# Optimization experiments

Hardware: AMD Instinct MI355X
Metric: run time of the kernel (lower is better)

The kernel has to match this reference:

```python
import jax, jax.numpy as jnp
import numpy as np

B, H, W, C, NH, WS, DEPTH = 32, 56, 56, 192, 6, 7, 2
SHIFTS = (0, WS // 2)
N = WS * WS
NW = (H // WS) * (W // WS)
HD = C // NH
SCALE = HD ** -0.5


def _rel_index():
    coords = np.stack(np.meshgrid(np.arange(WS), np.arange(WS), indexing='ij')).reshape(2, -1)
    rel = (coords[:, :, None] - coords[:, None, :]).transpose(1, 2, 0)
    rel[..., 0] += WS - 1
    rel[..., 1] += WS - 1
    rel[..., 0] *= 2 * WS - 1
    return jnp.asarray(rel.sum(-1))  # (N, N) int

REL_IDX = _rel_index()


def _attn_mask():
    # BasicLayer.creat_mask for the shifted block (shift = WS//2)
    img = np.zeros((H, W))
    sl = (slice(0, -WS), slice(-WS, -SHIFTS[1]), slice(-SHIFTS[1], None))
    cnt = 0
    for hs in sl:
        for ws_ in sl:
            img[hs, ws_] = cnt
            cnt += 1
    mw = img.reshape(H // WS, WS, W // WS, WS).transpose(0, 2, 1, 3).reshape(-1, N)
    d = mw[:, None, :] - mw[:, :, None]  # unsqueeze(1) - unsqueeze(2)
    return jnp.asarray(np.where(d != 0, -100.0, 0.0).astype(np.float32))  # (NW, N, N)

ATTN_MASK = _attn_mask()


def _ln(x, w, b):
    mu = x.mean(-1, keepdims=True)
    var = ((x - mu) ** 2).mean(-1, keepdims=True)
    return (x - mu) * jax.lax.rsqrt(var + 1e-5) * w + b


def _block(x, p, shift):
    Bn, L, Cc = x.shape
    shortcut = x
    h = _ln(x, p['n1w'], p['n1b']).reshape(Bn, H, W, Cc)
    if shift > 0:
        h = jnp.roll(h, (-shift, -shift), axis=(1, 2))
    # window_partition -> (Bn*NW, N, C)
    h = h.reshape(Bn, H // WS, WS, W // WS, WS, Cc).transpose(0, 1, 3, 2, 4, 5).reshape(-1, N, Cc)
    qkv = (h @ p['qkvw'].T + p['qkvb']).reshape(-1, N, 3, NH, HD).transpose(2, 0, 3, 1, 4)
    q, k, v = qkv[0] * SCALE, qkv[1], qkv[2]  # (Bw, NH, N, HD)
    attn = jnp.einsum('bhnd,bhmd->bhnm', q, k)
    bias = p['rpb'][REL_IDX].transpose(2, 0, 1)  # (NH, N, N)
    attn = attn + bias[None]
    if shift > 0:
        attn = attn.reshape(Bn, NW, NH, N, N) + ATTN_MASK[None, :, None]
        attn = attn.reshape(-1, NH, N, N)
    attn = jax.nn.softmax(attn, axis=-1)
    h = jnp.einsum('bhnm,bhmd->bhnd', attn, v).transpose(0, 2, 1, 3).reshape(-1, N, Cc)
    h = h @ p['projw'].T + p['projb']
    # window_reverse
    h = h.reshape(Bn, H // WS, W // WS, WS, WS, Cc).transpose(0, 1, 3, 2, 4, 5).reshape(Bn, H, W, Cc)
    if shift > 0:
        # NOTE: source rolls back by window_size (not shift_size); replicated faithfully
        h = jnp.roll(h, (WS, WS), axis=(1, 2))
    x = shortcut + h.reshape(Bn, L, Cc)
    m = _ln(x, p['n2w'], p['n2b'])
    m = jax.nn.gelu(m @ p['f1w'].T + p['f1b'], approximate=False) @ p['f2w'].T + p['f2b']
    return x + m


def setup_inputs() -> dict:
    key = jax.random.key(0)
    ks = jax.random.split(key, 15)
    r = lambda k, s, sc: jax.random.normal(k, s, dtype=jnp.float32) * sc
    return {
        'x': r(ks[0], (B, H * W, C), 1.0),
        'n1w': 1.0 + r(ks[1], (DEPTH, C), 0.01),
        'n1b': r(ks[2], (DEPTH, C), 0.01),
        'qkvw': r(ks[3], (DEPTH, 3 * C, C), 0.05),
        'qkvb': r(ks[4], (DEPTH, 3 * C), 0.01),
        'rpb': r(ks[5], (DEPTH, (2 * WS - 1) ** 2, NH), 0.02),
        'projw': r(ks[6], (DEPTH, C, C), 0.05),
        'projb': r(ks[7], (DEPTH, C), 0.01),
        'n2w': 1.0 + r(ks[8], (DEPTH, C), 0.01),
        'n2b': r(ks[9], (DEPTH, C), 0.01),
        'f1w': r(ks[10], (DEPTH, 4 * C, C), 0.05),
        'f1b': r(ks[11], (DEPTH, 4 * C), 0.01),
        'f2w': r(ks[12], (DEPTH, C, 4 * C), 0.05),
        'f2b': r(ks[13], (DEPTH, C), 0.01),
    }


def reference(x, n1w, n1b, qkvw, qkvb, rpb, projw, projb, n2w, n2b, f1w, f1b, f2w, f2b):
    for i in range(DEPTH):
        p = {'n1w': n1w[i], 'n1b': n1b[i], 'qkvw': qkvw[i], 'qkvb': qkvb[i],
             'rpb': rpb[i], 'projw': projw[i], 'projb': projb[i],
             'n2w': n2w[i], 'n2b': n2b[i], 'f1w': f1w[i], 'f1b': f1b[i],
             'f2w': f2w[i], 'f2b': f2b[i]}
        x = _block(x, p, SHIFTS[i])
    return x
```

## Files before the change

### kernel.cpp

```cpp
#include <hip/hip_runtime.h>
#include <hip/hip_bf16.h>
#include <math.h>

typedef __hip_bfloat16 bf16;

#define BB    32
#define HH    56
#define WWI   56
#define CC    192
#define NHH   6
#define WSS   7
#define NN    49
#define NWIN  64
#define HDD   32
#define LL    (HH*WWI)
#define ROWS  (BB*NWIN*NN)
#define TOT   ((size_t)ROWS*CC)
#define SCALEQ 0.17677669529663687f

#define OFF_N1W   0
#define OFF_N1B   384
#define OFF_QKVW  768
#define OFF_QKVB  221952
#define OFF_RPB   223104
#define OFF_PROJW 225132
#define OFF_PROJB 298860
#define OFF_N2W   299244
#define OFF_N2B   299628
#define OFF_F1W   300012
#define OFF_F1B   594924
#define OFF_F2W   596460
#define OFF_F2B   891372

typedef __bf16 bf16x8v __attribute__((ext_vector_type(8)));
typedef float  f32x4   __attribute__((ext_vector_type(4)));

__device__ __forceinline__ float tof(bf16 v){ return __bfloat162float(v); }
__device__ __forceinline__ bf16  tob(float v){ return __float2bfloat16(v); }
__device__ __forceinline__ float xload(const float* p){ return *p; }
__device__ __forceinline__ float xload(const bf16*  p){ return tof(*p); }
__device__ __forceinline__ void  xstore(float* p, float v){ *p = v; }
__device__ __forceinline__ void  xstore(bf16*  p, float v){ *p = tob(v); }

__device__ __forceinline__ bf16x8v ldfrag(const bf16* p){
    return *(const bf16x8v*)p;
}
__device__ __forceinline__ unsigned short bfbits(float v){
    bf16 b = tob(v);
    return __builtin_bit_cast(unsigned short, b);
}
__device__ __forceinline__ bf16 mkbf(unsigned short u){
    return __builtin_bit_cast(bf16, u);
}

__device__ __forceinline__ float fast_gelu(float x){
    float u = fabsf(x) * 0.70710678118f;
    float t = __builtin_amdgcn_rcpf(1.f + 0.3275911f*u);
    float p = t*(0.254829592f + t*(-0.284496736f + t*(1.421413741f +
              t*(-1.453152027f + t*1.061405429f))));
    float e = __expf(-u*u);
    float erfu = 1.f - p*e;
    float s = copysignf(erfu, x);
    return 0.5f*x*(1.f + s);
}

__global__ void k_detect(const unsigned short* __restrict__ w, int* __restrict__ flag){
    if (blockIdx.x == 0 && threadIdx.x == 0){
        int cnt = 0;
        for (int k = 0; k < 16; ++k){
            unsigned short u = w[2*k];
            if (u >= 0x3E00 && u <= 0x4100) ++cnt;
        }
        *flag = (cnt >= 8) ? 1 : 0;
    }
}

__global__ void k_canon(const void* __restrict__ src, bf16* __restrict__ dst,
                        int n, const int* __restrict__ flag){
    int i = blockIdx.x * blockDim.x + threadIdx.x;
    if (i >= n) return;
    if (*flag) dst[i] = ((const bf16*)src)[i];
    else       dst[i] = tob(((const float*)src)[i]);
}

template<typename XT>
__global__ void k_convert_in(const void* __restrict__ in, XT* __restrict__ X,
                             const int* __restrict__ flag){
    size_t i = (size_t)blockIdx.x * blockDim.x + threadIdx.x;
    if (i >= TOT) return;
    float v = (*flag) ? tof(((const bf16*)in)[i]) : ((const float*)in)[i];
    xstore(&X[i], v);
}

template<typename XT>
__global__ void k_out(const XT* __restrict__ X, void* __restrict__ out,
                      const int* __restrict__ flag){
    size_t i = (size_t)blockIdx.x * blockDim.x + threadIdx.x;
    if (i >= TOT) return;
    float v = xload(&X[i]);
    if (*flag) ((bf16*)out)[i] = tob(v);
    else       ((float*)out)[i] = v;
}

template<typename XT>
__global__ __launch_bounds__(256) void k_ln_part(const XT* __restrict__ X,
        const bf16* __restrict__ w, const bf16* __restrict__ bsh,
        bf16* __restrict__ Hwin, int shift){
    int wv = threadIdx.x >> 6, lane = threadIdx.x & 63;
    int row = blockIdx.x*4 + wv;
    int b   = row / (NWIN*NN);
    int win = (row / NN) % NWIN;
    int n   = row % NN;
    int wh = win >> 3, ww = win & 7;
    int iy = n / WSS, ix = n % WSS;
    int sy = (wh*WSS + iy + shift) % HH;
    int sx = (ww*WSS + ix + shift) % WWI;
    const XT* src = X + ((size_t)(b*LL + sy*WWI + sx))*CC;
    float v0 = xload(&src[lane]);
    float v1 = xload(&src[lane+64]);
    float v2 = xload(&src[lane+128]);
    float sm  = v0+v1+v2;
    float sm2 = v0*v0+v1*v1+v2*v2;
    #pragma unroll
    for (int st = 1; st < 64; st <<= 1){
        sm  += __shfl_xor(sm,  st);
        sm2 += __shfl_xor(sm2, st);
    }
    float mu  = sm * (1.f/CC);
    float inv = rsqrtf(sm2*(1.f/CC) - mu*mu + 1e-5f);
    bf16* dst = Hwin + (size_t)row*CC;
    dst[lane]     = tob((v0-mu)*inv*tof(w[lane])     + tof(bsh[lane]));
    dst[lane+64]  = tob((v1-mu)*inv*tof(w[lane+64])  + tof(bsh[lane+64]));
    dst[lane+128] = tob((v2-mu)*inv*tof(w[lane+128]) + tof(bsh[lane+128]));
}

__device__ __forceinline__ int mt0(int i){ return (i < 3) ? i*16 : 33; }

__global__ __launch_bounds__(512, 4) void k_attn(const bf16* __restrict__ Hwin,
        const bf16* __restrict__ qkvw, const bf16* __restrict__ qkvb,
        const bf16* __restrict__ rpb, bf16* __restrict__ AOut, int masked){
    __shared__ bf16 smem[31104];
    bf16* qls = smem;
    bf16* kls = smem + 9408;
    bf16* vT  = smem + 18816;
    bf16* Pls = smem;

    int t = threadIdx.x;
    int win  = blockIdx.x;
    int winl = win & (NWIN-1);
    int wh = winl >> 3, ww = winl & 7;
    int wv = t >> 6, lane = t & 63;
    int li16 = lane & 15, quad = lane >> 4;

    for (int idx = t; idx < 192*15; idx += 512){
        int d = idx / 15, tokp = 49 + idx % 15;
        vT[d*64 + (tokp ^ ((d&7)<<3))] = tob(0.f);
    }

    {
        int p = wv & 1, c = wv >> 1;
        int m0a = mt0(2*p), m0b = mt0(2*p+1);
        const bf16* hg = Hwin + (size_t)win*NN*CC;
        bf16x8v afa[6], afb[6];
        #pragma unroll
        for (int kc = 0; kc < 6; ++kc){
            afa[kc] = ldfrag(hg + (m0a+li16)*CC + kc*32 + quad*8);
            afb[kc] = ldfrag(hg + (m0b+li16)*CC + kc*32 + quad*8);
        }
        #pragma unroll 3
        for (int j = 0; j < 9; ++j){
            int nt = c + 4*j;
            int col = nt*16 + li16;
            f32x4 acc0 = {0.f,0.f,0.f,0.f}, acc1 = {0.f,0.f,0.f,0.f};
            #pragma unroll
            for (int kc = 0; kc < 6; ++kc){
                bf16x8v bfr = ldfrag(qkvw + (size_t)col*CC + kc*32 + quad*8);
                acc0 = __builtin_amdgcn_mfma_f32_16x16x32_bf16(afa[kc], bfr, acc0, 0, 0, 0);
                acc1 = __builtin_amdgcn_mfma_f32_16x16x32_bf16(afb[kc], bfr, acc1, 0, 0, 0);
            }
            float bias = tof(qkvb[col]);
            int m  = col / CC;
            int cm = col - m*CC;
            #pragma unroll
            for (int r = 0; r < 4; ++r){
                int rowA = m0a + quad*4 + r;
                int rowB = m0b + quad*4 + r;
                float v0 = acc0[r] + bias, v1 = acc1[r] + bias;
                if (m == 0){
                    qls[rowA*CC + (cm ^ ((rowA&7)<<3))] = tob(v0*SCALEQ);
                    qls[rowB*CC + (cm ^ ((rowB&7)<<3))] = tob(v1*SCALEQ);
                } else if (m == 1){
                    kls[rowA*CC + (cm ^ ((rowA&7)<<3))] = tob(v0);
                    kls[rowB*CC + (cm ^ ((rowB&7)<<3))] = tob(v1);
                } else {
                    vT[cm*64 + (rowA ^ ((cm&7)<<3))] = tob(v0);
                    vT[cm*64 + (rowB ^ ((cm&7)<<3))] = tob(v1);
                }
            }
        }
    }
    __syncthreads();

    unsigned int pk[3][8];
    #pragma unroll
    for (int j = 0; j < 3; ++j){
        int id = wv + 8*j;
        int mt = id & 3, h = id >> 2;
        int m0 = mt0(mt);
        int rowq = m0 + li16;
        bf16x8v afr = ldfrag(qls + rowq*CC + ((h*32 + quad*8) ^ ((rowq&7)<<3)));
        f32x4 s[4];
        #pragma unroll
        for (int nt = 0; nt < 4; ++nt){
            int rowk = nt*16 + li16;
            bf16x8v bfr = ldfrag(kls + rowk*CC + ((h*32 + quad*8) ^ ((rowk&7)<<3)));
            f32x4 z = {0.f,0.f,0.f,0.f};
            s[nt] = __builtin_amdgcn_mfma_f32_16x16x32_bf16(afr, bfr, z, 0, 0, 0);
        }
        #pragma unroll
        for (int nt = 0; nt < 4; ++nt){
            int jj = nt*16 + li16;
            int valid = (jj < NN);
            int jc = valid ? jj : 48;
            int yj = (jc*37) >> 8, xj = jc - 7*yj;
            int lj = 0;
            if (masked){
                int ayj = wh*WSS + yj, axj = ww*WSS + xj;
                lj = ((ayj<49)?0:(ayj<53)?1:2)*3 + ((axj<49)?0:(axj<53)?1:2);
            }
            #pragma unroll
            for (int r = 0; r < 4; ++r){
                int i = m0 + quad*4 + r;
                int yi = (i*37) >> 8, xi = i - 7*yi;
                int ridx = (yi - yj + 6)*13 + (xi - xj + 6);
                float v = s[nt][r] + tof(rpb[ridx*NHH + h]);
                if (masked){
                    int ayi = wh*WSS + yi, axi = ww*WSS + xi;
                    int li = ((ayi<49)?0:(ayi<53)?1:2)*3 + ((axi<49)?0:(axi<53)?1:2);
                    if (li != lj) v -= 100.f;
                }
                s[nt][r] = valid ? v : -1e30f;
            }
        }
        float mx[4], sm[4];
        #pragma unroll
        for (int r = 0; r < 4; ++r)
            mx[r] = fmaxf(fmaxf(s[0][r], s[1][r]), fmaxf(s[2][r], s[3][r]));
        #pragma unroll
        for (int st = 1; st < 16; st <<= 1){
            #pragma unroll
            for (int r = 0; r < 4; ++r) mx[r] = fmaxf(mx[r], __shfl_xor(mx[r], st));
        }
        #pragma unroll
        for (int nt = 0; nt < 4; ++nt){
            #pragma unroll
            for (int r = 0; r < 4; ++r) s[nt][r] = __expf(s[nt][r] - mx[r]);
        }
        #pragma unroll
        for (int r = 0; r < 4; ++r) sm[r] = (s[0][r]+s[1][r]) + (s[2][r]+s[3][r]);
        #pragma unroll
        for (int st = 1; st < 16; st <<= 1){
            #pragma unroll
            for (int r = 0; r < 4; ++r) sm[r] += __shfl_xor(sm[r], st);
        }
        #pragma unroll
        for (int r = 0; r < 4; ++r) sm[r] = 1.f / sm[r];
        #pragma unroll
        for (int nt = 0; nt < 4; ++nt){
            #pragma unroll
            for (int rr = 0; rr < 2; ++rr){
                unsigned int u0 = bfbits(s[nt][2*rr]   * sm[2*rr]);
                unsigned int u1 = bfbits(s[nt][2*rr+1] * sm[2*rr+1]);
                pk[j][nt*2+rr] = (u1 << 16) | u0;
            }
        }
    }
    __syncthreads();

    #pragma unroll
    for (int j = 0; j < 3; ++j){
        int id = wv + 8*j;
        int m0 = mt0(id & 3), h = id >> 2;
        #pragma unroll
        for (int nt = 0; nt < 4; ++nt){
            int jj = nt*16 + li16;
            #pragma unroll
            for (int rr = 0; rr < 2; ++rr){
                unsigned int u = pk[j][nt*2+rr];
                int tok0 = m0 + quad*4 + 2*rr;
                int tok1 = tok0 + 1;
                Pls[(h*NN + tok0)*64 + (jj ^ ((tok0&7)<<3))] = mkbf((unsigned short)(u & 0xffff));
                Pls[(h*NN + tok1)*64 + (jj ^ ((tok1&7)<<3))] = mkbf((unsigned short)(u >> 16));
            }
        }
    }
    __syncthreads();

    {
        int mt = wv & 3, nto = wv >> 2;
        int m0 = mt0(mt), n0 = nto*16;
        #pragma unroll
        for (int h = 0; h < NHH; ++h){
            f32x4 acc = {0.f,0.f,0.f,0.f};
            #pragma unroll
            for (int kc = 0; kc < 2; ++kc){
                int rowp = m0 + li16;
                bf16x8v afr = ldfrag(Pls + (h*NN + rowp)*64 + ((kc*32 + quad*8) ^ ((rowp&7)<<3)));
                int rowv = h*HDD + n0 + li16;
                bf16x8v bfr = ldfrag(vT + rowv*64 + ((kc*32 + quad*8) ^ ((rowv&7)<<3)));
                acc = __builtin_amdgcn_mfma_f32_16x16x32_bf16(afr, bfr, acc, 0, 0, 0);
            }
            #pragma unroll
            for (int r = 0; r < 4; ++r){
                int tok = m0 + quad*4 + r;
                AOut[(size_t)win*NN*CC + tok*CC + h*HDD + n0 + li16] = tob(acc[r]);
            }
        }
    }
}

#define AS_STRIDE 200
template<typename XT>
__global__ __launch_bounds__(256) void k_proj_res(const bf16* __restrict__ AOut,
        const bf16* __restrict__ pw, const bf16* __restrict__ pb,
        XT* __restrict__ X, int shift){
    __shared__ bf16 as[32*AS_STRIDE];
    int t = threadIdx.x;
    int row0 = blockIdx.x * 32;
    for (int idx = t; idx < 32*CC; idx += 256){
        int r = idx / CC, c = idx % CC;
        as[r*AS_STRIDE + c] = AOut[(size_t)(row0 + r)*CC + c];
    }
    __syncthreads();
    int wv = t >> 6, lane = t & 63;
    int li16 = lane & 15, quad = lane >> 4;
    int roll = (shift > 0) ? WSS : 0;
    for (int nt = 0; nt < 3; ++nt){
        int n0 = wv*48 + nt*16;
        int col = n0 + li16;
        bf16x8v bfr[6];
        #pragma unroll
        for (int kc = 0; kc < 6; ++kc)
            bfr[kc] = ldfrag(pw + (size_t)col*CC + kc*32 + quad*8);
        float bias = tof(pb[col]);
        for (int mt = 0; mt < 2; ++mt){
            int m0 = mt*16;
            f32x4 acc = {0.f,0.f,0.f,0.f};
            #pragma unroll
            for (int kc = 0; kc < 6; ++kc){
                bf16x8v afr = ldfrag(as + (m0 + li16)*AS_STRIDE + kc*32 + quad*8);
                acc = __builtin_amdgcn_mfma_f32_16x16x32_bf16(afr, bfr[kc], acc, 0, 0, 0);
            }
            #pragma unroll
            for (int r = 0; r < 4; ++r){
                int grow = row0 + m0 + quad*4 + r;
                int b   = grow / (NWIN*NN);
                int rem = grow % (NWIN*NN);
                int win = rem / NN;
                int n   = rem % NN;
                int wh = win >> 3, ww = win & 7;
                int iy = n / WSS, ix = n % WSS;
                int y = (wh*WSS + iy + roll) % HH;
                int x = (ww*WSS + ix + roll) % WWI;
                size_t idx = ((size_t)(b*LL + y*WWI + x))*CC + col;
                xstore(&X[idx], xload(&X[idx]) + acc[r] + bias);
            }
        }
    }
}

template<typename XT>
__global__ __launch_bounds__(256, 4) void k_mlp(XT* __restrict__ X,
        const bf16* __restrict__ n2w, const bf16* __restrict__ n2b,
        const bf16* __restrict__ w1, const bf16* __restrict__ b1,
        const bf16* __restrict__ w2, const bf16* __restrict__ b2){
    __shared__ bf16  xin[32*192];
    __shared__ bf16  h1h[32*384];
    __shared__ float part[256], part2[256];
    __shared__ float stats[64];
    int t = threadIdx.x;
    size_t row0 = (size_t)blockIdx.x * 32;

    float vals[24];
    int r8 = t >> 3, s8 = t & 7;
    {
        const XT* xr = X + (row0 + r8)*CC + s8*24;
        if constexpr (sizeof(XT) == 4){
            #pragma unroll
            for (int q = 0; q < 6; ++q){
                float4 f = *(const float4*)((const float*)xr + q*4);
                vals[q*4+0]=f.x; vals[q*4+1]=f.y; vals[q*4+2]=f.z; vals[q*4+3]=f.w;
            }
        } else {
            #pragma unroll
            for (int q = 0; q < 3; ++q){
                bf16x8v f = ldfrag((const bf16*)xr + q*8);
                #pragma unroll
                for (int e = 0; e < 8; ++e) vals[q*8+e] = tof(mkbf(__builtin_bit_cast(unsigned short, f[e])));
            }
        }
        float sm = 0.f, sm2 = 0.f;
        #pragma unroll
        for (int c = 0; c < 24; ++c){ sm += vals[c]; sm2 += vals[c]*vals[c]; }
        part[t] = sm; part2[t] = sm2;
    }
    __syncthreads();
    if (t < 32){
        float s = 0.f, s2 = 0.f;
        #pragma unroll
        for (int k = 0; k < 8; ++k){ s += part[t*8+k]; s2 += part2[t*8+k]; }
        float mu  = s * (1.f/CC);
        float var = s2 * (1.f/CC) - mu*mu;
        stats[t]      = mu;
        stats[32 + t] = rsqrtf(var + 1e-5f);
    }
    __syncthreads();
    {
        float mu = stats[r8], inv = stats[32+r8];
        #pragma unroll
        for (int c = 0; c < 24; ++c){
            int col = s8*24 + c;
            xin[r8*192 + (col ^ ((r8&7)<<3))] =
                tob((vals[c]-mu)*inv*tof(n2w[col]) + tof(n2b[col]));
        }
    }
    __syncthreads();

    int wv = t >> 6, lane = t & 63;
    int li16 = lane & 15, quad = lane >> 4;
    int sw = (li16 & 7) << 3;

    bf16x8v afr0[6], afr1[6];
    #pragma unroll
    for (int kc = 0; kc < 6; ++kc){
        afr0[kc] = ldfrag(xin + (0  + li16)*192 + ((kc*32 + quad*8) ^ sw));
        afr1[kc] = ldfrag(xin + (16 + li16)*192 + ((kc*32 + quad*8) ^ sw));
    }

    f32x4 acc2[3][2];
    #pragma unroll
    for (int nt = 0; nt < 3; ++nt){
        acc2[nt][0] = (f32x4){0.f,0.f,0.f,0.f};
        acc2[nt][1] = (f32x4){0.f,0.f,0.f,0.f};
    }

    #pragma unroll
    for (int half = 0; half < 2; ++half){
        #pragma unroll 2
        for (int nt6 = 0; nt6 < 6; ++nt6){
            int cl  = (wv*6 + nt6)*16 + li16;
            int col = half*384 + cl;
            bf16x8v bfr[6];
            #pragma unroll
            for (int kc = 0; kc < 6; ++kc)
                bfr[kc] = ldfrag(w1 + (size_t)col*CC + kc*32 + quad*8);
            float bb = tof(b1[col]);
            f32x4 acA = {0.f,0.f,0.f,0.f}, acB = {0.f,0.f,0.f,0.f};
            #pragma unroll
            for (int kc = 0; kc < 6; ++kc){
                acA = __builtin_amdgcn_mfma_f32_16x16x32_bf16(afr0[kc], bfr[kc], acA, 0, 0, 0);
                acB = __builtin_amdgcn_mfma_f32_16x16x32_bf16(afr1[kc], bfr[kc], acB, 0, 0, 0);
            }
            #pragma unroll
            for (int r = 0; r < 4; ++r){
                int rowA = quad*4 + r, rowB = 16 + quad*4 + r;
                h1h[rowA*384 + (cl ^ ((rowA&7)<<3))] = tob(fast_gelu(acA[r] + bb));
                h1h[rowB*384 + (cl ^ ((rowB&7)<<3))] = tob(fast_gelu(acB[r] + bb));
            }
        }
        __syncthreads();
        #pragma unroll 4
        for (int kc = 0; kc < 12; ++kc){
            int kg = half*12 + kc;
            bf16x8v a0 = ldfrag(h1h + (0  + li16)*384 + ((kc*32 + quad*8) ^ sw));
            bf16x8v a1 = ldfrag(h1h + (16 + li16)*384 + ((kc*32 + quad*8) ^ sw));
            #pragma unroll
            for (int nt = 0; nt < 3; ++nt){
                int col = wv*48 + nt*16 + li16;
                bf16x8v bfr = ldfrag(w2 + (size_t)col*768 + kg*32 + quad*8);
                acc2[nt][0] = __builtin_amdgcn_mfma_f32_16x16x32_bf16(a0, bfr, acc2[nt][0], 0, 0, 0);
                acc2[nt][1] = __builtin_amdgcn_mfma_f32_16x16x32_bf16(a1, bfr, acc2[nt][1], 0, 0, 0);
            }
        }
        __syncthreads();
    }

    #pragma unroll
    for (int nt = 0; nt < 3; ++nt){
        int col = wv*48 + nt*16 + li16;
        float bias = tof(b2[col]);
        #pragma unroll
        for (int r = 0; r < 4; ++r){
            size_t i0 = (row0 + 0  + quad*4 + r)*CC + col;
            size_t i1 = (row0 + 16 + quad*4 + r)*CC + col;
            xstore(&X[i0], xload(&X[i0]) + acc2[nt][0][r] + bias);
            xstore(&X[i1], xload(&X[i1]) + acc2[nt][1][r] + bias);
        }
    }
}

template<typename XT>
static void run_pipeline(const bf16* wb, const void* xin, int* flag,
                         XT* X, bf16* Hwin, bf16* AOut, void* out,
                         hipStream_t stream){
    k_convert_in<XT><<<(int)(TOT/256), 256, 0, stream>>>(xin, X, flag);
    for (int i = 0; i < 2; ++i){
        int shift = i ? (WSS/2) : 0;
        k_ln_part<XT><<<ROWS/4, 256, 0, stream>>>(X, wb+OFF_N1W + i*CC,
                wb+OFF_N1B + i*CC, Hwin, shift);
        k_attn<<<BB*NWIN, 512, 0, stream>>>(Hwin,
                wb+OFF_QKVW + (size_t)i*3*CC*CC, wb+OFF_QKVB + (size_t)i*3*CC,
                wb+OFF_RPB + (size_t)i*169*NHH, AOut, i);
        k_proj_res<XT><<<ROWS/32, 256, 0, stream>>>(AOut,
                wb+OFF_PROJW + (size_t)i*CC*CC, wb+OFF_PROJB + i*CC, X, shift);
        k_mlp<XT><<<ROWS/32, 256, 0, stream>>>(X,
                wb+OFF_N2W + i*CC, wb+OFF_N2B + i*CC,
                wb+OFF_F1W + (size_t)i*4*CC*CC, wb+OFF_F1B + (size_t)i*4*CC,
                wb+OFF_F2W + (size_t)i*CC*4*CC, wb+OFF_F2B + i*CC);
    }
    k_out<XT><<<(int)(TOT/256), 256, 0, stream>>>(X, out, flag);
}

extern "C" void kernel_launch(void* const* d_in, const int* in_sizes, int n_in,
                              void* d_out, int out_size, void* d_ws, size_t ws_size,
                              hipStream_t stream){
    char* p = (char*)d_ws;
    int*  flag = (int*)p;
    bf16* wb   = (bf16*)(p + 16);
    char* q    = p + 16 + (2u<<20);

    k_detect<<<1, 64, 0, stream>>>((const unsigned short*)d_in[1], flag);

    static const int widx[13] = {1,2,3,4,5,6,7,8,9,10,11,12,13};
    static const int woff[13] = {OFF_N1W,OFF_N1B,OFF_QKVW,OFF_QKVB,OFF_RPB,
                                 OFF_PROJW,OFF_PROJB,OFF_N2W,OFF_N2B,
                                 OFF_F1W,OFF_F1B,OFF_F2W,OFF_F2B};
    static const int wsz[13]  = {384,384,221184,1152,2028,73728,384,384,384,
                                 294912,1536,294912,384};
    for (int k = 0; k < 13; ++k)
        k_canon<<<(wsz[k]+255)/256, 256, 0, stream>>>(d_in[widx[k]], wb+woff[k],
                                                      wsz[k], flag);

    size_t needF32 = 16 + (2u<<20) + TOT*4 + TOT*2 + TOT*2;
    if (ws_size >= needF32){
        float* X   = (float*)q;       q += TOT*4;
        bf16* Hwin = (bf16*)q;        q += TOT*2;
        bf16* AOut = (bf16*)q;
        run_pipeline<float>(wb, d_in[0], flag, X, Hwin, AOut, d_out, stream);
    } else {
        bf16* X    = (bf16*)q;        q += TOT*2;
        bf16* Hwin = (bf16*)q;        q += TOT*2;
        bf16* AOut = (bf16*)q;
        run_pipeline<bf16>(wb, d_in[0], flag, X, Hwin, AOut, d_out, stream);
    }
}
```

Baseline: 1.202 ms.

## Retile fused MLP kernel to 64-row blocks with four hidden-dimension passes

The fused LayerNorm+MLP kernel now processes 64 rows per block instead of 32. The hidden dimension is split into four 192-wide passes, each staged through a 64x192 shared buffer. Every weight fragment loaded from global memory now feeds four MFMA row tiles instead of two, halving the weight traffic per row. LayerNorm is computed per wave with shuffle reductions instead of shared-memory partial sums. This costs more registers (accumulators are 3x4 per wave), a lower occupancy target, and half as many blocks in the grid.

```diff
diff --git a/kernel.cpp b/kernel.cpp
--- a/kernel.cpp
+++ b/kernel.cpp
@@ -370,131 +370,119 @@
 }
 
 template<typename XT>
-__global__ __launch_bounds__(256, 4) void k_mlp(XT* __restrict__ X,
+__global__ __launch_bounds__(256, 3) void k_mlp(XT* __restrict__ X,
         const bf16* __restrict__ n2w, const bf16* __restrict__ n2b,
         const bf16* __restrict__ w1, const bf16* __restrict__ b1,
         const bf16* __restrict__ w2, const bf16* __restrict__ b2){
-    __shared__ bf16  xin[32*192];
-    __shared__ bf16  h1h[32*384];
-    __shared__ float part[256], part2[256];
-    __shared__ float stats[64];
+    __shared__ bf16 xin[64*192];
+    __shared__ bf16 h1p[64*192];
     int t = threadIdx.x;
-    size_t row0 = (size_t)blockIdx.x * 32;
-
-    float vals[24];
-    int r8 = t >> 3, s8 = t & 7;
-    {
-        const XT* xr = X + (row0 + r8)*CC + s8*24;
-        if constexpr (sizeof(XT) == 4){
-            #pragma unroll
-            for (int q = 0; q < 6; ++q){
-                float4 f = *(const float4*)((const float*)xr + q*4);
-                vals[q*4+0]=f.x; vals[q*4+1]=f.y; vals[q*4+2]=f.z; vals[q*4+3]=f.w;
-            }
-        } else {
-            #pragma unroll
-            for (int q = 0; q < 3; ++q){
-                bf16x8v f = ldfrag((const bf16*)xr + q*8);
-                #pragma unroll
-                for (int e = 0; e < 8; ++e) vals[q*8+e] = tof(mkbf(__builtin_bit_cast(unsigned short, f[e])));
-            }
-        }
-        float sm = 0.f, sm2 = 0.f;
-        #pragma unroll
-        for (int c = 0; c < 24; ++c){ sm += vals[c]; sm2 += vals[c]*vals[c]; }
-        part[t] = sm; part2[t] = sm2;
-    }
-    __syncthreads();
-    if (t < 32){
-        float s = 0.f, s2 = 0.f;
-        #pragma unroll
-        for (int k = 0; k < 8; ++k){ s += part[t*8+k]; s2 += part2[t*8+k]; }
-        float mu  = s * (1.f/CC);
-        float var = s2 * (1.f/CC) - mu*mu;
-        stats[t]      = mu;
-        stats[32 + t] = rsqrtf(var + 1e-5f);
-    }
-    __syncthreads();
-    {
-        float mu = stats[r8], inv = stats[32+r8];
-        #pragma unroll
-        for (int c = 0; c < 24; ++c){
-            int col = s8*24 + c;
-            xin[r8*192 + (col ^ ((r8&7)<<3))] =
-                tob((vals[c]-mu)*inv*tof(n2w[col]) + tof(n2b[col]));
-        }
-    }
-    __syncthreads();
-
     int wv = t >> 6, lane = t & 63;
     int li16 = lane & 15, quad = lane >> 4;
+    size_t row0 = (size_t)blockIdx.x * 64;
+
+    {
+        float nw0 = tof(n2w[lane]), nw1 = tof(n2w[lane+64]), nw2 = tof(n2w[lane+128]);
+        float nb0 = tof(n2b[lane]), nb1 = tof(n2b[lane+64]), nb2 = tof(n2b[lane+128]);
+        #pragma unroll 4
+        for (int i = 0; i < 16; ++i){
+            int r = wv*16 + i;
+            const XT* xr = X + (row0 + r)*CC;
+            float v0 = xload(&xr[lane]);
+            float v1 = xload(&xr[lane+64]);
+            float v2 = xload(&xr[lane+128]);
+            float sm  = v0+v1+v2;
+            float sm2 = v0*v0+v1*v1+v2*v2;
+            #pragma unroll
+            for (int st = 1; st < 64; st <<= 1){
+                sm  += __shfl_xor(sm,  st);
+                sm2 += __shfl_xor(sm2, st);
+            }
+            float mu  = sm * (1.f/CC);
+            float inv = rsqrtf(sm2*(1.f/CC) - mu*mu + 1e-5f);
+            int swz = (r&7)<<3;
+            bf16* xrow = xin + r*192;
+            xrow[lane        ^ swz] = tob((v0-mu)*inv*nw0 + nb0);
+            xrow[(lane+64)   ^ swz] = tob((v1-mu)*inv*nw1 + nb1);
+            xrow[(lane+128)  ^ swz] = tob((v2-mu)*inv*nw2 + nb2);
+        }
+    }
+    __syncthreads();
+
     int sw = (li16 & 7) << 3;
-
-    bf16x8v afr0[6], afr1[6];
+    f32x4 acc2[3][4];
     #pragma unroll
-    for (int kc = 0; kc < 6; ++kc){
-        afr0[kc] = ldfrag(xin + (0  + li16)*192 + ((kc*32 + quad*8) ^ sw));
-        afr1[kc] = ldfrag(xin + (16 + li16)*192 + ((kc*32 + quad*8) ^ sw));
-    }
-
-    f32x4 acc2[3][2];
+    for (int j = 0; j < 3; ++j)
+        #pragma unroll
+        for (int m = 0; m < 4; ++m)
+            acc2[j][m] = (f32x4){0.f,0.f,0.f,0.f};
+
+    for (int pass = 0; pass < 4; ++pass){
+        f32x4 a1[3][4];
+        #pragma unroll
+        for (int j = 0; j < 3; ++j)
+            #pragma unroll
+            for (int m = 0; m < 4; ++m)
+                a1[j][m] = (f32x4){0.f,0.f,0.f,0.f};
+        #pragma unroll
+        for (int kc = 0; kc < 6; ++kc){
+            bf16x8v af[4];
+            #pragma unroll
+            for (int m = 0; m < 4; ++m)
+                af[m] = ldfrag(xin + (m*16 + li16)*192 + ((kc*32 + quad*8) ^ sw));
+            #pragma unroll
+            for (int j = 0; j < 3; ++j){
+                int col = pass*192 + (wv*3 + j)*16 + li16;
+                bf16x8v bfr = ldfrag(w1 + (size_t)col*CC + kc*32 + quad*8);
+                #pragma unroll
+                for (int m = 0; m < 4; ++m)
+                    a1[j][m] = __builtin_amdgcn_mfma_f32_16x16x32_bf16(af[m], bfr, a1[j][m], 0, 0, 0);
+            }
+        }
+        #pragma unroll
+        for (int j = 0; j < 3; ++j){
+            int cl = (wv*3 + j)*16 + li16;
+            float bb = tof(b1[pass*192 + cl]);
+            #pragma unroll
+            for (int m = 0; m < 4; ++m){
+                #pragma unroll
+                for (int r = 0; r < 4; ++r){
+                    int row = m*16 + quad*4 + r;
+                    h1p[row*192 + (cl ^ ((row&7)<<3))] = tob(fast_gelu(a1[j][m][r] + bb));
+                }
+            }
+        }
+        __syncthreads();
+        #pragma unroll
+        for (int kc = 0; kc < 6; ++kc){
+            bf16x8v af[4];
+            #pragma unroll
+            for (int m = 0; m < 4; ++m)
+                af[m] = ldfrag(h1p + (m*16 + li16)*192 + ((kc*32 + quad*8) ^ sw));
+            int kg = pass*6 + kc;
+            #pragma unroll
+            for (int j = 0; j < 3; ++j){
+                int col = wv*48 + j*16 + li16;
+                bf16x8v bfr = ldfrag(w2 + (size_t)col*768 + kg*32 + quad*8);
+                #pragma unroll
+                for (int m = 0; m < 4; ++m)
+                    acc2[j][m] = __builtin_amdgcn_mfma_f32_16x16x32_bf16(af[m], bfr, acc2[j][m], 0, 0, 0);
+            }
+        }
+        __syncthreads();
+    }
+
     #pragma unroll
-    for (int nt = 0; nt < 3; ++nt){
-        acc2[nt][0] = (f32x4){0.f,0.f,0.f,0.f};
-        acc2[nt][1] = (f32x4){0.f,0.f,0.f,0.f};
-    }
-
-    #pragma unroll
-    for (int half = 0; half < 2; ++half){
-        #pragma unroll 2
-        for (int nt6 = 0; nt6 < 6; ++nt6){
-            int cl  = (wv*6 + nt6)*16 + li16;
-            int col = half*384 + cl;
-            bf16x8v bfr[6];
-            #pragma unroll
-            for (int kc = 0; kc < 6; ++kc)
-                bfr[kc] = ldfrag(w1 + (size_t)col*CC + kc*32 + quad*8);
-            float bb = tof(b1[col]);
-            f32x4 acA = {0.f,0.f,0.f,0.f}, acB = {0.f,0.f,0.f,0.f};
-            #pragma unroll
-            for (int kc = 0; kc < 6; ++kc){
-                acA = __builtin_amdgcn_mfma_f32_16x16x32_bf16(afr0[kc], bfr[kc], acA, 0, 0, 0);
-                acB = __builtin_amdgcn_mfma_f32_16x16x32_bf16(afr1[kc], bfr[kc], acB, 0, 0, 0);
-            }
+    for (int j = 0; j < 3; ++j){
+        int col = wv*48 + j*16 + li16;
+        float bias = tof(b2[col]);
+        #pragma unroll
+        for (int m = 0; m < 4; ++m){
             #pragma unroll
             for (int r = 0; r < 4; ++r){
-                int rowA = quad*4 + r, rowB = 16 + quad*4 + r;
-                h1h[rowA*384 + (cl ^ ((rowA&7)<<3))] = tob(fast_gelu(acA[r] + bb));
-                h1h[rowB*384 + (cl ^ ((rowB&7)<<3))] = tob(fast_gelu(acB[r] + bb));
-            }
-        }
-        __syncthreads();
-        #pragma unroll 4
-        for (int kc = 0; kc < 12; ++kc){
-            int kg = half*12 + kc;
-            bf16x8v a0 = ldfrag(h1h + (0  + li16)*384 + ((kc*32 + quad*8) ^ sw));
-            bf16x8v a1 = ldfrag(h1h + (16 + li16)*384 + ((kc*32 + quad*8) ^ sw));
-            #pragma unroll
-            for (int nt = 0; nt < 3; ++nt){
-                int col = wv*48 + nt*16 + li16;
-                bf16x8v bfr = ldfrag(w2 + (size_t)col*768 + kg*32 + quad*8);
-                acc2[nt][0] = __builtin_amdgcn_mfma_f32_16x16x32_bf16(a0, bfr, acc2[nt][0], 0, 0, 0);
-                acc2[nt][1] = __builtin_amdgcn_mfma_f32_16x16x32_bf16(a1, bfr, acc2[nt][1], 0, 0, 0);
-            }
-        }
-        __syncthreads();
-    }
-
-    #pragma unroll
-    for (int nt = 0; nt < 3; ++nt){
-        int col = wv*48 + nt*16 + li16;
-        float bias = tof(b2[col]);
-        #pragma unroll
-        for (int r = 0; r < 4; ++r){
-            size_t i0 = (row0 + 0  + quad*4 + r)*CC + col;
-            size_t i1 = (row0 + 16 + quad*4 + r)*CC + col;
-            xstore(&X[i0], xload(&X[i0]) + acc2[nt][0][r] + bias);
-            xstore(&X[i1], xload(&X[i1]) + acc2[nt][1][r] + bias);
+                size_t idx = (row0 + m*16 + quad*4 + r)*CC + col;
+                xstore(&X[idx], xload(&X[idx]) + acc2[j][m][r] + bias);
+            }
         }
     }
 }
@@ -513,7 +501,7 @@
                 wb+OFF_RPB + (size_t)i*169*NHH, AOut, i);
         k_proj_res<XT><<<ROWS/32, 256, 0, stream>>>(AOut,
                 wb+OFF_PROJW + (size_t)i*CC*CC, wb+OFF_PROJB + i*CC, X, shift);
-        k_mlp<XT><<<ROWS/32, 256, 0, stream>>>(X,
+        k_mlp<XT><<<ROWS/64, 256, 0, stream>>>(X,
                 wb+OFF_N2W + i*CC, wb+OFF_N2B + i*CC,
                 wb+OFF_F1W + (size_t)i*4*CC*CC, wb+OFF_F1B + (size_t)i*4*CC,
                 wb+OFF_F2W + (size_t)i*CC*4*CC, wb+OFF_F2B + i*CC);
```

Measured after the change: 1.376 ms. +14.4%, slower.
